# Kernel optimization log

Measured on AMD Instinct MI355X. Metric: run time of the kernel, lower is better.

The kernel has to match this reference:

```python
import jax, jax.numpy as jnp
from jax import lax
import numpy as np

B, DIM, HF, H, W, P = 4, 64, 128, 256, 256, 8  # patch_size = 8


def setup_inputs() -> dict:
    key = jax.random.key(0)
    k0, k1, k2, k3, k4 = jax.random.split(key, 5)
    C2 = 2 * HF
    x = jax.random.normal(k0, (B, DIM, H, W), dtype=jnp.float32)
    w_in = jax.random.normal(k1, (C2, DIM), dtype=jnp.float32) * 0.05      # 1x1 conv weight
    w_dw = jax.random.normal(k2, (C2, 1, 3, 3), dtype=jnp.float32) * 0.1   # depthwise 3x3
    fft_filt = 1.0 + 0.1 * jax.random.normal(k3, (C2, 1, 1, P, P // 2 + 1), dtype=jnp.float32)
    w_out = jax.random.normal(k4, (DIM, HF), dtype=jnp.float32) * 0.05     # 1x1 conv weight
    return {"x": x, "w_in": w_in, "w_dw": w_dw, "fft_filt": fft_filt, "w_out": w_out}


def reference(x, w_in, w_dw, fft_filt, w_out):
    # project_in: 1x1 conv (no bias)
    h = jnp.einsum('oc,bchw->bohw', w_in, x)
    b, c, hh, ww = h.shape
    # b c (h p1) (w p2) -> b c h w p1 p2
    hp = h.reshape(b, c, hh // P, P, ww // P, P).transpose(0, 1, 2, 4, 3, 5)
    # patchwise spectral gating
    f = jnp.fft.rfft2(hp.astype(jnp.float32)) * fft_filt
    hp = jnp.fft.irfft2(f, s=(P, P))
    # b c h w p1 p2 -> b c (h p1) (w p2)
    h = hp.transpose(0, 1, 2, 4, 3, 5).reshape(b, c, hh, ww)
    # depthwise 3x3 conv, SAME padding, groups = channels
    h = lax.conv_general_dilated(h, w_dw, (1, 1), 'SAME',
                                 feature_group_count=c,
                                 dimension_numbers=('NCHW', 'OIHW', 'NCHW'))
    x1, x2 = jnp.split(h, 2, axis=1)
    g = jax.nn.gelu(x1, approximate=False) * x2
    # project_out: 1x1 conv
    return jnp.einsum('oc,bchw->bohw', w_out, g)
```

## Files before the change

kernel.cpp:

```cpp
#include <hip/hip_runtime.h>
#include <hip/hip_bf16.h>

#define NB 4
#define DIMC 64
#define C2 256
#define HFC 128
#define HH 256
#define WW 256
#define HW (HH * WW)

typedef __attribute__((ext_vector_type(8))) short short8;
typedef __attribute__((ext_vector_type(4))) float f32x4;

__device__ __forceinline__ f32x4 mfma16(short8 a, short8 b, f32x4 c) {
  return __builtin_amdgcn_mfma_f32_16x16x32_bf16(a, b, c, 0, 0, 0);
}

__device__ __forceinline__ short f2bs(float f) {
  __hip_bfloat16 h = __float2bfloat16(f);
  union { __hip_bfloat16 h; short s; } u; u.h = h;
  return u.s;
}

__device__ __forceinline__ float bs2f(short s) {
  union { float f; unsigned u; } v;
  v.u = ((unsigned)(unsigned short)s) << 16;
  return v.f;
}

__device__ __forceinline__ float fast_gelu(float u) {
  float au = fabsf(u);
  float z = au * 0.70710678118654752f;
  float e = __expf(-z * z);
  float t = __builtin_amdgcn_rcpf(fmaf(0.3275911f, z, 1.0f));
  float p = fmaf(t, 1.061405429f, -1.453152027f);
  p = fmaf(t, p, 1.421413741f);
  p = fmaf(t, p, -0.284496736f);
  p = fmaf(t, p, 0.254829592f);
  p *= t;
  return fmaxf(u, 0.f) - 0.5f * au * p * e;
}

__global__ __launch_bounds__(64) void prep_kernel(
    const float* __restrict__ w_in, const float* __restrict__ fft,
    const float* __restrict__ w_out, __hip_bfloat16* __restrict__ A1,
    __hip_bfloat16* __restrict__ A2, __hip_bfloat16* __restrict__ Mf) {
  int blk = blockIdx.x;
  int l = threadIdx.x;
  int mm = l & 15, qj = l >> 4;
  if (blk < C2) {
    __shared__ float Feff[64];
    __shared__ float kc[64];
    __shared__ float ct[8];
    if (l < 8) {
      const float s = 0.70710678118654752f;
      const float v0[8] = {1.f, s, 0.f, -s, -1.f, -s, 0.f, s};
      ct[l] = v0[l];
    }
    int c = blk;
    const float* f = fft + c * 40;
    int u = l >> 3, v = l & 7;
    int um = (8 - u) & 7;
    float val;
    if (v <= 4) {
      val = f[u * 5 + v];
      if (v == 0 || v == 4) val = 0.5f * (val + f[um * 5 + v]);
    } else {
      val = f[um * 5 + (8 - v)];
    }
    Feff[l] = val;
    __syncthreads();
    int dy = l >> 3, dx = l & 7;
    float s = 0.f;
    for (int uu = 0; uu < 8; ++uu)
      for (int vv = 0; vv < 8; ++vv)
        s += Feff[uu * 8 + vv] * ct[(uu * dy + vv * dx) & 7];
    kc[l] = s * (1.f / 64.f);
    __syncthreads();
    for (int mb = 0; mb < 4; ++mb) {
      int p = mb * 16 + mm;
      int py = p >> 3, px = p & 7;
      for (int kb = 0; kb < 2; ++kb)
        for (int j = 0; j < 8; ++j) {
          int q = kb * 32 + qj * 8 + j;
          int qy = q >> 3, qx = q & 7;
          float kv = kc[((py - qy) & 7) * 8 + ((px - qx) & 7)];
          Mf[(size_t)c * 4096 + (size_t)((mb * 2 + kb) * 64 + l) * 8 + j] =
              __float2bfloat16(kv);
        }
    }
  } else if (blk == C2) {
    for (int mb = 0; mb < 16; ++mb)
      for (int kb = 0; kb < 2; ++kb)
        for (int j = 0; j < 8; ++j) {
          int m = mb * 16 + mm, k = kb * 32 + qj * 8 + j;
          A1[(size_t)((mb * 2 + kb) * 64 + l) * 8 + j] =
              __float2bfloat16(w_in[m * 64 + k]);
        }
  } else {
    for (int mb = 0; mb < 4; ++mb)
      for (int kb = 0; kb < 4; ++kb)
        for (int j = 0; j < 8; ++j) {
          int m = mb * 16 + mm, k = kb * 32 + qj * 8 + j;
          A2[(size_t)((mb * 4 + kb) * 64 + l) * 8 + j] =
              __float2bfloat16(w_out[m * 128 + k]);
        }
  }
}

#define FS_LDS_BYTES 81920

__device__ __forceinline__ int hs_idx(int cL, int row, int patch, int qx) {
  int p2 = patch ^ ((cL >> 2) << 1) ^ row;
  return 32768 + cL * 512 + row * 64 + p2 * 8 + qx;
}

__device__ __forceinline__ void load_mf(short8* dst, const short8* Mfv, int c,
                                        int l) {
#pragma unroll
  for (int f = 0; f < 8; ++f) dst[f] = Mfv[(size_t)c * 512 + f * 64 + l];
}

__device__ __forceinline__ void spec_one(short* lds, const short8* mf, int cL,
                                         int cg, int g, int nn16, int l,
                                         __hip_bfloat16* hb, int Py, int x0) {
  int p8 = l & 7;
  short8 bs0 = *reinterpret_cast<const short8*>(&lds[hs_idx(cL, g, p8, 0)]);
  short8 bs1 = *reinterpret_cast<const short8*>(&lds[hs_idx(cL, 4 + g, p8, 0)]);
  f32x4 accs[4];
#pragma unroll
  for (int mb = 0; mb < 4; ++mb) {
    accs[mb] = (f32x4){0.f, 0.f, 0.f, 0.f};
    accs[mb] = mfma16(mf[mb * 2 + 0], bs0, accs[mb]);
    accs[mb] = mfma16(mf[mb * 2 + 1], bs1, accs[mb]);
  }
  int slot = 32768 + cL * 512;
  if (nn16 < 8) {
#pragma unroll
    for (int mb = 0; mb < 4; ++mb)
#pragma unroll
      for (int r = 0; r < 4; ++r) {
        int p = mb * 16 + g * 4 + r;
        lds[slot + (p >> 3) * 64 + nn16 * 8 + (p & 7)] = f2bs(accs[mb][r]);
      }
  }
  asm volatile("s_waitcnt lgkmcnt(0)" ::: "memory");
  short8 ov = *reinterpret_cast<const short8*>(&lds[slot + l * 8]);
  __hip_bfloat16* hp = hb + (size_t)cg * HW +
                       (size_t)(Py * 8 + (l >> 3)) * WW + x0 + (l & 7) * 8;
  *reinterpret_cast<short8*>(hp) = ov;
}

__global__ __launch_bounds__(256, 2) void fs_kernel(
    const float* __restrict__ x, const __hip_bfloat16* __restrict__ A1,
    const __hip_bfloat16* __restrict__ Mf, __hip_bfloat16* __restrict__ h) {
  extern __shared__ char smem[];
  short* lds = reinterpret_cast<short*>(smem);
  int pg = blockIdx.x, b = blockIdx.y;
  int Py = pg >> 2, x0 = (pg & 3) * 64;
  int t = threadIdx.x;
  int w = t >> 6, l = t & 63;
  int g = l >> 4;
  int nn16 = l & 15;

  const short8* A1v = reinterpret_cast<const short8*>(A1);
  const short8* Mfv = reinterpret_cast<const short8*>(Mf);
  __hip_bfloat16* hb = h + (size_t)b * C2 * HW;

  short8 afA0 = A1v[0 * 64 + l];
  short8 afA1 = A1v[1 * 64 + l];
  short8 mfA[8], mfB[8];
  load_mf(mfA, Mfv, w * 4, l);

  {
    int n = t & 63, dgrp = t >> 6;
    int nblk = n >> 4, nn = n & 15;
#pragma unroll
    for (int py = 0; py < 8; ++py) {
      const float* xb =
          x + (size_t)b * DIMC * HW + (size_t)(Py * 8 + py) * WW + x0 + n;
#pragma unroll
      for (int s = 0; s < 2; ++s) {
        int jb = dgrp + s * 4;
        int kb = jb >> 2, quad = jb & 3;
        short8 pk;
#pragma unroll
        for (int j = 0; j < 8; ++j) pk[j] = f2bs(xb[(size_t)(jb * 8 + j) * HW]);
        *reinterpret_cast<short8*>(
            &lds[(size_t)(py * 512 + (kb * 4 + nblk) * 64 + quad * 16 + nn) * 8]) = pk;
      }
    }
  }
  __syncthreads();

  const short8* xv = reinterpret_cast<const short8*>(lds);

  for (int i = 0; i < 16; ++i) {
#pragma unroll
    for (int py2 = 0; py2 < 2; ++py2) {
      int py = w * 2 + py2;
#pragma unroll
      for (int nb = 0; nb < 4; ++nb) {
        short8 b0 = xv[py * 512 + (0 * 4 + nb) * 64 + l];
        short8 b1 = xv[py * 512 + (1 * 4 + nb) * 64 + l];
        f32x4 acc = (f32x4){0.f, 0.f, 0.f, 0.f};
        acc = mfma16(afA0, b0, acc);
        acc = mfma16(afA1, b1, acc);
        int xc = nb * 16 + nn16;
#pragma unroll
        for (int r = 0; r < 4; ++r) {
          int cL = g * 4 + r;
          lds[hs_idx(cL, py, xc >> 3, xc & 7)] = f2bs(acc[r]);
        }
      }
    }
    int inx = (i + 1) & 15;
    short8 afN0 = A1v[(inx * 2 + 0) * 64 + l];
    short8 afN1 = A1v[(inx * 2 + 1) * 64 + l];
    __syncthreads();

    int c0 = i * 16 + w * 4;
    load_mf(mfB, Mfv, c0 + 1, l);
    spec_one(lds, mfA, w * 4 + 0, c0 + 0, g, nn16, l, hb, Py, x0);
    load_mf(mfA, Mfv, c0 + 2, l);
    spec_one(lds, mfB, w * 4 + 1, c0 + 1, g, nn16, l, hb, Py, x0);
    load_mf(mfB, Mfv, c0 + 3, l);
    spec_one(lds, mfA, w * 4 + 2, c0 + 2, g, nn16, l, hb, Py, x0);
    load_mf(mfA, Mfv, inx * 16 + w * 4, l);
    spec_one(lds, mfB, w * 4 + 3, c0 + 3, g, nn16, l, hb, Py, x0);
    __syncthreads();

    afA0 = afN0;
    afA1 = afN1;
  }
}

__global__ __launch_bounds__(256) void dwgelu_kernel(
    const __hip_bfloat16* __restrict__ h2, const float* __restrict__ w_dw,
    __hip_bfloat16* __restrict__ gf) {
  __shared__ short ldsJ[8 * 1024];
  int jb = blockIdx.x;
  int y0 = blockIdx.y * 4;
  int b = blockIdx.z;
  int t = threadIdx.x;
  int j = t >> 5, xg = t & 31;
  int x0 = xg * 8;
  int c1 = jb * 8 + j, c2 = c1 + HFC;
  const __hip_bfloat16* hbase = h2 + (size_t)b * C2 * HW;

  float wd1[9], wd2[9];
#pragma unroll
  for (int k = 0; k < 9; ++k) {
    wd1[k] = w_dw[c1 * 9 + k];
    wd2[k] = w_dw[c2 * 9 + k];
  }

  float acc1[4][8], acc2[4][8];
#pragma unroll
  for (int r = 0; r < 4; ++r)
#pragma unroll
    for (int i = 0; i < 8; ++i) { acc1[r][i] = 0.f; acc2[r][i] = 0.f; }

#pragma unroll
  for (int ir = -1; ir <= 4; ++ir) {
    int yy = y0 + ir;
    bool valid = (yy >= 0) && (yy < HH);
    float f1[10], f2[10];
    if (valid) {
      const __hip_bfloat16* r1 = hbase + ((size_t)c1 * HH + yy) * WW;
      const __hip_bfloat16* r2 = hbase + ((size_t)c2 * HH + yy) * WW;
      short8 v1 = *reinterpret_cast<const short8*>(r1 + x0);
      short8 v2 = *reinterpret_cast<const short8*>(r2 + x0);
#pragma unroll
      for (int i = 0; i < 8; ++i) { f1[i + 1] = bs2f(v1[i]); f2[i + 1] = bs2f(v2[i]); }
      f1[0] = (x0 > 0) ? __bfloat162float(r1[x0 - 1]) : 0.f;
      f2[0] = (x0 > 0) ? __bfloat162float(r2[x0 - 1]) : 0.f;
      f1[9] = (x0 + 8 < WW) ? __bfloat162float(r1[x0 + 8]) : 0.f;
      f2[9] = (x0 + 8 < WW) ? __bfloat162float(r2[x0 + 8]) : 0.f;
    } else {
#pragma unroll
      for (int i = 0; i < 10; ++i) { f1[i] = 0.f; f2[i] = 0.f; }
    }
#pragma unroll
    for (int dy = -1; dy <= 1; ++dy) {
      int r = ir - dy;
      if (r < 0 || r >= 4) continue;
      int ky = dy + 1;
#pragma unroll
      for (int i = 0; i < 8; ++i) {
        acc1[r][i] += f1[i] * wd1[ky * 3] + f1[i + 1] * wd1[ky * 3 + 1] +
                      f1[i + 2] * wd1[ky * 3 + 2];
        acc2[r][i] += f2[i] * wd2[ky * 3] + f2[i + 1] * wd2[ky * 3 + 1] +
                      f2[i + 2] * wd2[ky * 3 + 2];
      }
    }
  }

#pragma unroll
  for (int r = 0; r < 4; ++r) {
    short8 pk;
#pragma unroll
    for (int i = 0; i < 8; ++i) {
      float gg = fast_gelu(acc1[r][i]);
      pk[i] = f2bs(gg * acc2[r][i]);
    }
    *reinterpret_cast<short8*>(&ldsJ[j * 1024 + r * 256 + x0]) = pk;
  }
  __syncthreads();

  int kb = jb >> 2, quad = jb & 3;
  short8* gfv = reinterpret_cast<short8*>(gf) + (size_t)b * 1048576;
#pragma unroll
  for (int k = 0; k < 4; ++k) {
    short8 v;
#pragma unroll
    for (int j2 = 0; j2 < 8; ++j2) v[j2] = ldsJ[j2 * 1024 + k * 256 + t];
    int pix = (y0 + k) * WW + t;
    gfv[((size_t)(pix >> 4) * 4 + kb) * 64 + quad * 16 + (pix & 15)] = v;
  }
}

__global__ __launch_bounds__(256) void gemm2_kernel(
    const __hip_bfloat16* __restrict__ gf, const __hip_bfloat16* __restrict__ A2,
    float* __restrict__ out) {
  int b = blockIdx.y;
  int pix0 = blockIdx.x * 256;
  int tid = threadIdx.x;
  int w = tid >> 6, l = tid & 63;
  int quad = l >> 4, ln = l & 15;
  const short8* A2v = reinterpret_cast<const short8*>(A2);
  short8 af[4][4];
#pragma unroll
  for (int mb = 0; mb < 4; ++mb)
#pragma unroll
    for (int kb = 0; kb < 4; ++kb) af[mb][kb] = A2v[(mb * 4 + kb) * 64 + l];
  const short8* gv = reinterpret_cast<const short8*>(gf) + (size_t)b * 1048576;
  f32x4 acc[4][4];
#pragma unroll
  for (int i = 0; i < 4; ++i)
#pragma unroll
    for (int j = 0; j < 4; ++j) acc[i][j] = (f32x4){0.f, 0.f, 0.f, 0.f};
#pragma unroll
  for (int nb = 0; nb < 4; ++nb) {
    size_t pixblk = (size_t)blockIdx.x * 16 + w * 4 + nb;
    short8 bf[4];
#pragma unroll
    for (int kb = 0; kb < 4; ++kb) bf[kb] = gv[(pixblk * 4 + kb) * 64 + l];
#pragma unroll
    for (int mb = 0; mb < 4; ++mb)
#pragma unroll
      for (int kb = 0; kb < 4; ++kb)
        acc[mb][nb] = mfma16(af[mb][kb], bf[kb], acc[mb][nb]);
  }
#pragma unroll
  for (int mb = 0; mb < 4; ++mb)
#pragma unroll
    for (int nb = 0; nb < 4; ++nb)
#pragma unroll
      for (int r = 0; r < 4; ++r) {
        int o = mb * 16 + quad * 4 + r;
        int pix = pix0 + w * 64 + nb * 16 + ln;
        out[((size_t)b * DIMC + o) * HW + pix] = acc[mb][nb][r];
      }
}

extern "C" void kernel_launch(void* const* d_in, const int* in_sizes, int n_in,
                              void* d_out, int out_size, void* d_ws,
                              size_t ws_size, hipStream_t stream) {
  const float* x = (const float*)d_in[0];
  const float* w_in = (const float*)d_in[1];
  const float* w_dw = (const float*)d_in[2];
  const float* fft = (const float*)d_in[3];
  const float* w_out = (const float*)d_in[4];
  float* out = (float*)d_out;
  char* ws = (char*)d_ws;
  __hip_bfloat16* A1 = (__hip_bfloat16*)(ws);
  __hip_bfloat16* A2 = (__hip_bfloat16*)(ws + 32768);
  __hip_bfloat16* Mf = (__hip_bfloat16*)(ws + 49152);
  __hip_bfloat16* gf = (__hip_bfloat16*)(ws + 2146304);
  __hip_bfloat16* h = (__hip_bfloat16*)(ws + 69255168);

  static bool fs_attr_set = false;
  if (!fs_attr_set) {
    (void)hipFuncSetAttribute((const void*)fs_kernel,
                              hipFuncAttributeMaxDynamicSharedMemorySize,
                              FS_LDS_BYTES);
    fs_attr_set = true;
  }

  prep_kernel<<<258, 64, 0, stream>>>(w_in, fft, w_out, A1, A2, Mf);
  fs_kernel<<<dim3(128, NB), 256, FS_LDS_BYTES, stream>>>(x, A1, Mf, h);
  dwgelu_kernel<<<dim3(16, 64, NB), 256, 0, stream>>>(h, w_dw, gf);
  gemm2_kernel<<<dim3(256, NB), 256, 0, stream>>>(gf, A2, out);
}
```

Baseline: 260.3 us.

## Halve fs_kernel tile width to raise occupancy and pair spectral stores

The fused projection+spectral kernel now handles 4 patches (32 columns) per block instead of 8. This halves LDS use to 40KB, raises launch bounds to 4 blocks per CU and doubles the grid, which should give more parallelism and better latency hiding. The spectral stage is split into a compute step and a paired store, so each lane writes one 16-byte chunk covering two channels. In exchange, the MFMA work per sync is halved, the 16x16 tile has half its N columns unused, and the swizzle pattern changes, which may bring back bank conflicts.

```diff
diff --git a/kernel.cpp b/kernel.cpp
--- a/kernel.cpp
+++ b/kernel.cpp
@@ -108,11 +108,12 @@
   }
 }
 
-#define FS_LDS_BYTES 81920
-
-__device__ __forceinline__ int hs_idx(int cL, int row, int patch, int qx) {
-  int p2 = patch ^ ((cL >> 2) << 1) ^ row;
-  return 32768 + cL * 512 + row * 64 + p2 * 8 + qx;
+#define FS_LDS_BYTES 40960
+#define HSB 16384
+
+__device__ __forceinline__ int hs_idx4(int cL, int row, int patch, int qx) {
+  int p2 = (patch ^ (cL >> 2) ^ row) & 3;
+  return HSB + cL * 256 + row * 32 + p2 * 8 + qx;
 }
 
 __device__ __forceinline__ void load_mf(short8* dst, const short8* Mfv, int c,
@@ -121,12 +122,12 @@
   for (int f = 0; f < 8; ++f) dst[f] = Mfv[(size_t)c * 512 + f * 64 + l];
 }
 
-__device__ __forceinline__ void spec_one(short* lds, const short8* mf, int cL,
-                                         int cg, int g, int nn16, int l,
-                                         __hip_bfloat16* hb, int Py, int x0) {
-  int p8 = l & 7;
-  short8 bs0 = *reinterpret_cast<const short8*>(&lds[hs_idx(cL, g, p8, 0)]);
-  short8 bs1 = *reinterpret_cast<const short8*>(&lds[hs_idx(cL, 4 + g, p8, 0)]);
+__device__ __forceinline__ void spec_compute_stage(short* lds, const short8* mf,
+                                                   int cL, int g, int nn16,
+                                                   int l) {
+  int p4 = l & 3;
+  short8 bs0 = *reinterpret_cast<const short8*>(&lds[hs_idx4(cL, g, p4, 0)]);
+  short8 bs1 = *reinterpret_cast<const short8*>(&lds[hs_idx4(cL, 4 + g, p4, 0)]);
   f32x4 accs[4];
 #pragma unroll
   for (int mb = 0; mb < 4; ++mb) {
@@ -134,30 +135,37 @@
     accs[mb] = mfma16(mf[mb * 2 + 0], bs0, accs[mb]);
     accs[mb] = mfma16(mf[mb * 2 + 1], bs1, accs[mb]);
   }
-  int slot = 32768 + cL * 512;
-  if (nn16 < 8) {
+  int slot = HSB + cL * 256;
+  if (nn16 < 4) {
 #pragma unroll
     for (int mb = 0; mb < 4; ++mb)
 #pragma unroll
       for (int r = 0; r < 4; ++r) {
         int p = mb * 16 + g * 4 + r;
-        lds[slot + (p >> 3) * 64 + nn16 * 8 + (p & 7)] = f2bs(accs[mb][r]);
+        lds[slot + (p >> 3) * 32 + nn16 * 8 + (p & 7)] = f2bs(accs[mb][r]);
       }
   }
+}
+
+__device__ __forceinline__ void spec_store_pair(short* lds, int cL0, int cg0,
+                                                int l, __hip_bfloat16* hb,
+                                                int Py, int x0) {
   asm volatile("s_waitcnt lgkmcnt(0)" ::: "memory");
-  short8 ov = *reinterpret_cast<const short8*>(&lds[slot + l * 8]);
-  __hip_bfloat16* hp = hb + (size_t)cg * HW +
-                       (size_t)(Py * 8 + (l >> 3)) * WW + x0 + (l & 7) * 8;
+  int ch = l >> 5, row = (l >> 2) & 7, ck = l & 3;
+  short8 ov = *reinterpret_cast<const short8*>(
+      &lds[HSB + (cL0 + ch) * 256 + row * 32 + ck * 8]);
+  __hip_bfloat16* hp = hb + (size_t)(cg0 + ch) * HW +
+                       (size_t)(Py * 8 + row) * WW + x0 + ck * 8;
   *reinterpret_cast<short8*>(hp) = ov;
 }
 
-__global__ __launch_bounds__(256, 2) void fs_kernel(
+__global__ __launch_bounds__(256, 4) void fs_kernel(
     const float* __restrict__ x, const __hip_bfloat16* __restrict__ A1,
     const __hip_bfloat16* __restrict__ Mf, __hip_bfloat16* __restrict__ h) {
   extern __shared__ char smem[];
   short* lds = reinterpret_cast<short*>(smem);
   int pg = blockIdx.x, b = blockIdx.y;
-  int Py = pg >> 2, x0 = (pg & 3) * 64;
+  int Py = pg >> 3, x0 = (pg & 7) * 32;
   int t = threadIdx.x;
   int w = t >> 6, l = t & 63;
   int g = l >> 4;
@@ -173,22 +181,19 @@
   load_mf(mfA, Mfv, w * 4, l);
 
   {
-    int n = t & 63, dgrp = t >> 6;
+    int jb = t >> 5;
+    int n = t & 31;
+    int kb = jb >> 2, quad = jb & 3;
     int nblk = n >> 4, nn = n & 15;
 #pragma unroll
     for (int py = 0; py < 8; ++py) {
       const float* xb =
           x + (size_t)b * DIMC * HW + (size_t)(Py * 8 + py) * WW + x0 + n;
-#pragma unroll
-      for (int s = 0; s < 2; ++s) {
-        int jb = dgrp + s * 4;
-        int kb = jb >> 2, quad = jb & 3;
-        short8 pk;
-#pragma unroll
-        for (int j = 0; j < 8; ++j) pk[j] = f2bs(xb[(size_t)(jb * 8 + j) * HW]);
-        *reinterpret_cast<short8*>(
-            &lds[(size_t)(py * 512 + (kb * 4 + nblk) * 64 + quad * 16 + nn) * 8]) = pk;
-      }
+      short8 pk;
+#pragma unroll
+      for (int j = 0; j < 8; ++j) pk[j] = f2bs(xb[(size_t)(jb * 8 + j) * HW]);
+      *reinterpret_cast<short8*>(
+          &lds[(size_t)(py * 256 + (kb * 2 + nblk) * 64 + quad * 16 + nn) * 8]) = pk;
     }
   }
   __syncthreads();
@@ -200,9 +205,9 @@
     for (int py2 = 0; py2 < 2; ++py2) {
       int py = w * 2 + py2;
 #pragma unroll
-      for (int nb = 0; nb < 4; ++nb) {
-        short8 b0 = xv[py * 512 + (0 * 4 + nb) * 64 + l];
-        short8 b1 = xv[py * 512 + (1 * 4 + nb) * 64 + l];
+      for (int nb = 0; nb < 2; ++nb) {
+        short8 b0 = xv[py * 256 + (0 * 2 + nb) * 64 + l];
+        short8 b1 = xv[py * 256 + (1 * 2 + nb) * 64 + l];
         f32x4 acc = (f32x4){0.f, 0.f, 0.f, 0.f};
         acc = mfma16(afA0, b0, acc);
         acc = mfma16(afA1, b1, acc);
@@ -210,7 +215,7 @@
 #pragma unroll
         for (int r = 0; r < 4; ++r) {
           int cL = g * 4 + r;
-          lds[hs_idx(cL, py, xc >> 3, xc & 7)] = f2bs(acc[r]);
+          lds[hs_idx4(cL, py, xc >> 3, xc & 7)] = f2bs(acc[r]);
         }
       }
     }
@@ -221,13 +226,15 @@
 
     int c0 = i * 16 + w * 4;
     load_mf(mfB, Mfv, c0 + 1, l);
-    spec_one(lds, mfA, w * 4 + 0, c0 + 0, g, nn16, l, hb, Py, x0);
+    spec_compute_stage(lds, mfA, w * 4 + 0, g, nn16, l);
     load_mf(mfA, Mfv, c0 + 2, l);
-    spec_one(lds, mfB, w * 4 + 1, c0 + 1, g, nn16, l, hb, Py, x0);
+    spec_compute_stage(lds, mfB, w * 4 + 1, g, nn16, l);
+    spec_store_pair(lds, w * 4 + 0, c0 + 0, l, hb, Py, x0);
     load_mf(mfB, Mfv, c0 + 3, l);
-    spec_one(lds, mfA, w * 4 + 2, c0 + 2, g, nn16, l, hb, Py, x0);
+    spec_compute_stage(lds, mfA, w * 4 + 2, g, nn16, l);
     load_mf(mfA, Mfv, inx * 16 + w * 4, l);
-    spec_one(lds, mfB, w * 4 + 3, c0 + 3, g, nn16, l, hb, Py, x0);
+    spec_compute_stage(lds, mfB, w * 4 + 3, g, nn16, l);
+    spec_store_pair(lds, w * 4 + 2, c0 + 2, l, hb, Py, x0);
     __syncthreads();
 
     afA0 = afN0;
@@ -389,7 +396,7 @@
   }
 
   prep_kernel<<<258, 64, 0, stream>>>(w_in, fft, w_out, A1, A2, Mf);
-  fs_kernel<<<dim3(128, NB), 256, FS_LDS_BYTES, stream>>>(x, A1, Mf, h);
+  fs_kernel<<<dim3(256, NB), 256, FS_LDS_BYTES, stream>>>(x, A1, Mf, h);
   dwgelu_kernel<<<dim3(16, 64, NB), 256, 0, stream>>>(h, w_dw, gf);
   gemm2_kernel<<<dim3(256, NB), 256, 0, stream>>>(gf, A2, out);
 }
```

Measured after the change: 307.3 us. 1.18x slower.
